# Optimization experiments

Measured on AMD Instinct MI355X. Metric: run time of the kernel, lower is better.

## Reference

```python
import jax, jax.numpy as jnp
import numpy as np

EMBED_DIM = 512
PAIR_DIM = 64
NUM_HEAD = 32
HEAD_DIM = EMBED_DIM // NUM_HEAD
LN_EPS = 1e-5


def layer_norm(x, gamma, beta):
    mu = jnp.mean(x, axis=-1, keepdims=True)
    var = jnp.var(x, axis=-1, keepdims=True)
    return (x - mu) * jax.lax.rsqrt(var + LN_EPS) * gamma + beta


def setup_inputs() -> dict:
    key = jax.random.key(0)
    ks = jax.random.split(key, 12)
    nc, n = 4, 512
    inp = {
        "query": jax.random.normal(ks[0], (nc, n, EMBED_DIM), dtype=jnp.float32),
        "pair": jax.random.normal(ks[1], (nc, n, n, PAIR_DIM), dtype=jnp.float32),
        "delta_pos": jax.random.normal(ks[2], (nc, n, n, 3), dtype=jnp.float32),
        # learned params
        "ln_q_g": jnp.ones((EMBED_DIM,), jnp.float32),
        "ln_q_b": jnp.zeros((EMBED_DIM,), jnp.float32),
        "ln_p_g": jnp.ones((PAIR_DIM,), jnp.float32),
        "ln_p_b": jnp.zeros((PAIR_DIM,), jnp.float32),
        # torch Linear weight layout [out, in]
        "Wq": jax.random.normal(ks[3], (EMBED_DIM, EMBED_DIM), jnp.float32) * (EMBED_DIM ** -0.5),
        "Wk": jax.random.normal(ks[4], (EMBED_DIM, EMBED_DIM), jnp.float32) * (EMBED_DIM ** -0.5),
        "Wv": jax.random.normal(ks[5], (EMBED_DIM, EMBED_DIM), jnp.float32) * (EMBED_DIM ** -0.5),
        "Wb": jax.random.normal(ks[6], (NUM_HEAD, PAIR_DIM), jnp.float32) * (PAIR_DIM ** -0.5),
        "bb": jnp.zeros((NUM_HEAD,), jnp.float32),
        # force_proj uses 'final' init (zeros); use small random so grads are nontrivial
        "Wf": jax.random.normal(ks[7], (1, EMBED_DIM), jnp.float32) * (EMBED_DIM ** -0.5),
    }
    return inp


def reference(query, pair, delta_pos, ln_q_g, ln_q_b, ln_p_g, ln_p_b, Wq, Wk, Wv, Wb, bb, Wf):
    nc, n, _ = query.shape
    H, D = NUM_HEAD, HEAD_DIM
    scaling = D ** -0.5

    xq = layer_norm(query, ln_q_g, ln_q_b)           # [c, n, E]
    xp = layer_norm(pair, ln_p_g, ln_p_b)            # [c, n, n, P]

    q = (xq @ Wq.T).reshape(nc, n, H, D).transpose(0, 2, 1, 3) * scaling  # [c,h,n,d]
    k = (xq @ Wk.T).reshape(nc, n, H, D).transpose(0, 2, 1, 3)            # [c,h,n,d]
    v = (xq @ Wv.T).reshape(nc, n, H, D).transpose(0, 2, 1, 3)            # [c,h,n,d]

    attn = jnp.einsum('chid,chjd->chij', q, k)                            # [c,h,n,n]
    bias = jnp.einsum('cijp,hp->chij', xp, Wb) + bb[None, :, None, None]  # [c,h,n,n]
    probs = jax.nn.softmax(attn + bias, axis=-1)  # dropout omitted (eval mode)

    # x[c,i,r,h,d] = sum_j probs[c,h,i,j] * delta_pos[c,i,j,r] * v[c,h,j,d]
    x = jnp.einsum('chij,cijr,chjd->cirhd', probs, delta_pos, v)
    x = x.reshape(nc, n, 3, H * D)                                        # [c,n,3,E]
    force = jnp.einsum('cire,e->cir', x, Wf[0])                           # [c,n,3]
    return force
```

## Files before the change

kernel.cpp:

```cpp
#include <hip/hip_runtime.h>
#include <hip/hip_bf16.h>
#include <math.h>

#define NN 512
#define HH 32
#define PP 64
#define EE 512

__global__ __launch_bounds__(256)
void prep_kernel(const float* __restrict__ Wv, const float* __restrict__ Wf,
                 const float* __restrict__ Wb, const float* __restrict__ pg,
                 const float* __restrict__ pb, const float* __restrict__ bbv,
                 float* __restrict__ Wu, float* __restrict__ Wbp,
                 float* __restrict__ s1, float* __restrict__ s2) {
    const int h = blockIdx.x;
    const int t = threadIdx.x;
    __shared__ float sh1[64], sh2[64];
#pragma unroll
    for (int r = 0; r < 2; ++r) {
        const int e = r * 256 + t;
        float acc = 0.f;
#pragma unroll
        for (int d = 0; d < 16; ++d)
            acc += Wf[h * 16 + d] * Wv[(size_t)(h * 16 + d) * EE + e];
        Wu[h * EE + e] = acc;
    }
    if (t < 64) {
        const float wb = Wb[h * PP + t];
        Wbp[h * PP + t] = pg[t] * wb;
        sh1[t] = pg[t] * wb;
        sh2[t] = pb[t] * wb;
    }
    __syncthreads();
    if (t == 0) {
        float a = 0.f, s = 0.f;
#pragma unroll
        for (int p = 0; p < 64; ++p) { a += sh1[p]; s += sh2[p]; }
        s1[h] = a;
        s2[h] = s + bbv[h];
    }
}

__global__ __launch_bounds__(256)
void ln_query_kernel(const float* __restrict__ x, const float* __restrict__ g,
                     const float* __restrict__ b, float* __restrict__ xq) {
    const int row = blockIdx.x;
    const int t = threadIdx.x;
    const int wave = t >> 6, lane = t & 63;
    const float2 v = ((const float2*)(x + (size_t)row * EE))[t];
    float s = v.x + v.y;
    float ss = v.x * v.x + v.y * v.y;
#pragma unroll
    for (int o = 32; o > 0; o >>= 1) {
        s += __shfl_xor(s, o, 64);
        ss += __shfl_xor(ss, o, 64);
    }
    __shared__ float rs[4], rss[4];
    if (lane == 0) { rs[wave] = s; rss[wave] = ss; }
    __syncthreads();
    s = rs[0] + rs[1] + rs[2] + rs[3];
    ss = rss[0] + rss[1] + rss[2] + rss[3];
    const float mu = s * (1.f / 512.f);
    const float var = ss * (1.f / 512.f) - mu * mu;
    const float istd = rsqrtf(var + 1e-5f);
    const float2 gg = ((const float2*)g)[t];
    const float2 bb2 = ((const float2*)b)[t];
    float2 o;
    o.x = (v.x - mu) * istd * gg.x + bb2.x;
    o.y = (v.y - mu) * istd * gg.y + bb2.y;
    ((float2*)(xq + (size_t)row * EE))[t] = o;
}

__global__ __launch_bounds__(256)
void proj_gemm_kernel(const float* __restrict__ xq, const float* __restrict__ Wq,
                      const float* __restrict__ Wk, const float* __restrict__ Wu,
                      float* __restrict__ qo, float* __restrict__ kt,
                      float* __restrict__ uT) {
    __shared__ float As[32][33];
    __shared__ float Bs[32][33];
    const int t = threadIdx.x;
    const int row0 = blockIdx.x * 32;
    const int col0 = blockIdx.y * 32;
    const int tx = t & 15, ty = t >> 4;
    const int lr = t >> 3;
    const int lk4 = (t & 7) * 4;

    const int gcb = col0 + lr;
    const float* wrow;
    if (gcb < 512) wrow = Wq + (size_t)gcb * EE;
    else if (gcb < 1024) wrow = Wk + (size_t)(gcb - 512) * EE;
    else wrow = Wu + (size_t)(gcb - 1024) * EE;
    const float* arow = xq + (size_t)(row0 + lr) * EE;

    float a00 = 0.f, a01 = 0.f, a10 = 0.f, a11 = 0.f;
#pragma unroll 1
    for (int k0 = 0; k0 < EE; k0 += 32) {
        const float4 av = *(const float4*)(arow + k0 + lk4);
        const float4 bv = *(const float4*)(wrow + k0 + lk4);
        __syncthreads();
        As[lk4 + 0][lr] = av.x; As[lk4 + 1][lr] = av.y;
        As[lk4 + 2][lr] = av.z; As[lk4 + 3][lr] = av.w;
        Bs[lk4 + 0][lr] = bv.x; Bs[lk4 + 1][lr] = bv.y;
        Bs[lk4 + 2][lr] = bv.z; Bs[lk4 + 3][lr] = bv.w;
        __syncthreads();
#pragma unroll
        for (int kk = 0; kk < 32; ++kk) {
            const float2 a = *(const float2*)&As[kk][ty * 2];
            const float2 b = *(const float2*)&Bs[kk][tx * 2];
            a00 += a.x * b.x; a01 += a.x * b.y;
            a10 += a.y * b.x; a11 += a.y * b.y;
        }
    }

    float accv[2][2] = {{a00, a01}, {a10, a11}};
#pragma unroll
    for (int r = 0; r < 2; ++r) {
        const int grow = row0 + ty * 2 + r;
        const int c = grow >> 9, n = grow & 511;
#pragma unroll
        for (int cc = 0; cc < 2; ++cc) {
            const int gc = col0 + tx * 2 + cc;
            const float v = accv[r][cc];
            if (gc < 512) {
                qo[(size_t)grow * EE + gc] = v * 0.25f;
            } else if (gc < 1024) {
                const int e = gc - 512;
                const int h = e >> 4, d = e & 15;
                kt[((((size_t)c * HH + h) * 8 + (d >> 1)) * NN + n) * 2 + (d & 1)] = v;
            } else {
                const int h = gc - 1024;
                uT[((size_t)c * HH + h) * NN + n] = v;
            }
        }
    }
}

__global__ __launch_bounds__(512)
void attn_force_kernel(const float* __restrict__ pair, const float* __restrict__ delta,
                       const float* __restrict__ qws, const float* __restrict__ kt,
                       const float* __restrict__ uT, const float* __restrict__ Wbp,
                       const float* __restrict__ s1, const float* __restrict__ s2,
                       float* __restrict__ out) {
    __shared__ float attn[HH][NN];
    __shared__ float invd[HH];
    __shared__ float red[8][3];

    const int t = threadIdx.x;
    const int wave = t >> 6, lane = t & 63;
    const int bid = blockIdx.x;
    const int c = bid >> 9;
    const int i = bid & 511;
    const int j = t;

    const float4* prow = (const float4*)(pair + (((size_t)c * NN + i) * NN + j) * PP);
    const float* qrow = qws + (size_t)bid * EE;
    const float2* ktc = (const float2*)(kt + (size_t)c * HH * 8 * NN * 2);

    float mu = 0.f, istd = 0.f;
#pragma unroll 1
    for (int g = 0; g < 4; ++g) {
        float l8[8] = {0.f, 0.f, 0.f, 0.f, 0.f, 0.f, 0.f, 0.f};
        float s = 0.f, ss = 0.f;
#pragma unroll
        for (int x = 0; x < 16; ++x) {
            const float4 pv = prow[x];
            if (g == 0) {
                s += pv.x + pv.y + pv.z + pv.w;
                ss += pv.x * pv.x + pv.y * pv.y + pv.z * pv.z + pv.w * pv.w;
            }
#pragma unroll
            for (int hh = 0; hh < 8; ++hh) {
                const float4 w = *(const float4*)(Wbp + (g * 8 + hh) * PP + x * 4);
                l8[hh] += pv.x * w.x + pv.y * w.y + pv.z * w.z + pv.w * w.w;
            }
        }
        if (g == 0) {
            mu = s * (1.f / 64.f);
            const float var = ss * (1.f / 64.f) - mu * mu;
            istd = rsqrtf(var + 1e-5f);
        }
#pragma unroll
        for (int hh = 0; hh < 8; ++hh) {
            const int h = g * 8 + hh;
            float qk = 0.f;
#pragma unroll
            for (int dp = 0; dp < 8; ++dp) {
                const float2 kv = ktc[((size_t)h * 8 + dp) * NN + j];
                const float2 qv = *(const float2*)(qrow + h * 16 + dp * 2);
                qk += kv.x * qv.x + kv.y * qv.y;
            }
            attn[h][j] = __expf(qk + istd * (l8[hh] - mu * s1[h]) + s2[h]);
        }
    }
    __syncthreads();

#pragma unroll
    for (int q = 0; q < 4; ++q) {
        const int h = wave * 4 + q;
        float v = 0.f;
#pragma unroll
        for (int x = 0; x < 8; ++x) v += attn[h][x * 64 + lane];
#pragma unroll
        for (int o = 32; o > 0; o >>= 1) v += __shfl_xor(v, o, 64);
        if (lane == 0) invd[h] = 1.f / v;
    }
    __syncthreads();

    float w = 0.f;
#pragma unroll
    for (int h = 0; h < HH; ++h)
        w += attn[h][j] * invd[h] * uT[((size_t)c * HH + h) * NN + j];

    const float* d3 = delta + (((size_t)c * NN + i) * NN + j) * 3;
    float fx = w * d3[0], fy = w * d3[1], fz = w * d3[2];
#pragma unroll
    for (int o = 32; o > 0; o >>= 1) {
        fx += __shfl_xor(fx, o, 64);
        fy += __shfl_xor(fy, o, 64);
        fz += __shfl_xor(fz, o, 64);
    }
    if (lane == 0) { red[wave][0] = fx; red[wave][1] = fy; red[wave][2] = fz; }
    __syncthreads();
    if (t == 0) {
        float ox = 0.f, oy = 0.f, oz = 0.f;
#pragma unroll
        for (int w8 = 0; w8 < 8; ++w8) { ox += red[w8][0]; oy += red[w8][1]; oz += red[w8][2]; }
        out[(size_t)bid * 3 + 0] = ox;
        out[(size_t)bid * 3 + 1] = oy;
        out[(size_t)bid * 3 + 2] = oz;
    }
}

extern "C" void kernel_launch(void* const* d_in, const int* in_sizes, int n_in,
                              void* d_out, int out_size, void* d_ws, size_t ws_size,
                              hipStream_t stream) {
    const float* query   = (const float*)d_in[0];
    const float* pair    = (const float*)d_in[1];
    const float* delta   = (const float*)d_in[2];
    const float* ln_q_g  = (const float*)d_in[3];
    const float* ln_q_b  = (const float*)d_in[4];
    const float* ln_p_g  = (const float*)d_in[5];
    const float* ln_p_b  = (const float*)d_in[6];
    const float* Wq      = (const float*)d_in[7];
    const float* Wk      = (const float*)d_in[8];
    const float* Wv      = (const float*)d_in[9];
    const float* Wb      = (const float*)d_in[10];
    const float* bbv     = (const float*)d_in[11];
    const float* Wf      = (const float*)d_in[12];
    float* out = (float*)d_out;

    float* ws = (float*)d_ws;
    float* xq  = ws;
    float* qws = xq + 2048 * 512;
    float* kt  = qws + 2048 * 512;
    float* uT  = kt + 2048 * 512;
    float* Wu  = uT + 4 * 32 * 512;
    float* Wbp = Wu + 32 * 512;
    float* s1  = Wbp + 32 * 64;
    float* s2  = s1 + 32;

    prep_kernel<<<32, 256, 0, stream>>>(Wv, Wf, Wb, ln_p_g, ln_p_b, bbv,
                                        Wu, Wbp, s1, s2);
    ln_query_kernel<<<2048, 256, 0, stream>>>(query, ln_q_g, ln_q_b, xq);
    proj_gemm_kernel<<<dim3(64, 33), 256, 0, stream>>>(xq, Wq, Wk, Wu,
                                                       qws, kt, uT);
    attn_force_kernel<<<2048, 512, 0, stream>>>(pair, delta, qws, kt, uT,
                                                Wbp, s1, s2, out);
}
```

Before: 590.6 us.

## Keep attention exponentials in registers and relayout K for float4 loads

The per-row attention exponentials now stay in a 32-entry register array, so the 64 KB shared-memory attention buffer is gone. The softmax denominator is built with wave shuffles and a small per-wave partial table. K is rewritten as contiguous 16-float rows per (head, key) so each thread can read it with four float4 loads, and the group loop is fully unrolled with a launch-bounds occupancy hint. The aim is higher occupancy from lower LDS use. The cost is more register pressure, and K reads are now strided across lanes (64 bytes apart), which may hurt coalescing.

Measured after the change: 1.898 ms. 221% more time.

```diff
diff --git a/kernel.cpp b/kernel.cpp
--- a/kernel.cpp
+++ b/kernel.cpp
@@ -74,7 +74,7 @@
 __global__ __launch_bounds__(256)
 void proj_gemm_kernel(const float* __restrict__ xq, const float* __restrict__ Wq,
                       const float* __restrict__ Wk, const float* __restrict__ Wu,
-                      float* __restrict__ qo, float* __restrict__ kt,
+                      float* __restrict__ qo, float* __restrict__ ktn,
                       float* __restrict__ uT) {
     __shared__ float As[32][33];
     __shared__ float Bs[32][33];
@@ -126,7 +126,7 @@
             } else if (gc < 1024) {
                 const int e = gc - 512;
                 const int h = e >> 4, d = e & 15;
-                kt[((((size_t)c * HH + h) * 8 + (d >> 1)) * NN + n) * 2 + (d & 1)] = v;
+                ktn[(((size_t)c * HH + h) * NN + n) * 16 + d] = v;
             } else {
                 const int h = gc - 1024;
                 uT[((size_t)c * HH + h) * NN + n] = v;
@@ -135,13 +135,13 @@
     }
 }
 
-__global__ __launch_bounds__(512)
+__global__ __launch_bounds__(512, 4)
 void attn_force_kernel(const float* __restrict__ pair, const float* __restrict__ delta,
-                       const float* __restrict__ qws, const float* __restrict__ kt,
+                       const float* __restrict__ qws, const float* __restrict__ ktn,
                        const float* __restrict__ uT, const float* __restrict__ Wbp,
                        const float* __restrict__ s1, const float* __restrict__ s2,
                        float* __restrict__ out) {
-    __shared__ float attn[HH][NN];
+    __shared__ float part[HH][8];
     __shared__ float invd[HH];
     __shared__ float red[8][3];
 
@@ -154,13 +154,15 @@
 
     const float4* prow = (const float4*)(pair + (((size_t)c * NN + i) * NN + j) * PP);
     const float* qrow = qws + (size_t)bid * EE;
-    const float2* ktc = (const float2*)(kt + (size_t)c * HH * 8 * NN * 2);
-
+    const float* ktb = ktn + (size_t)c * HH * NN * 16;
+
+    float e32[32];
     float mu = 0.f, istd = 0.f;
-#pragma unroll 1
+    float s = 0.f, ss = 0.f;
+
+#pragma unroll
     for (int g = 0; g < 4; ++g) {
         float l8[8] = {0.f, 0.f, 0.f, 0.f, 0.f, 0.f, 0.f, 0.f};
-        float s = 0.f, ss = 0.f;
 #pragma unroll
         for (int x = 0; x < 16; ++x) {
             const float4 pv = prow[x];
@@ -170,8 +172,8 @@
             }
 #pragma unroll
             for (int hh = 0; hh < 8; ++hh) {
-                const float4 w = *(const float4*)(Wbp + (g * 8 + hh) * PP + x * 4);
-                l8[hh] += pv.x * w.x + pv.y * w.y + pv.z * w.z + pv.w * w.w;
+                const float4 wv = *(const float4*)(Wbp + (g * 8 + hh) * PP + x * 4);
+                l8[hh] += pv.x * wv.x + pv.y * wv.y + pv.z * wv.z + pv.w * wv.w;
             }
         }
         if (g == 0) {
@@ -182,34 +184,41 @@
 #pragma unroll
         for (int hh = 0; hh < 8; ++hh) {
             const int h = g * 8 + hh;
-            float qk = 0.f;
-#pragma unroll
-            for (int dp = 0; dp < 8; ++dp) {
-                const float2 kv = ktc[((size_t)h * 8 + dp) * NN + j];
-                const float2 qv = *(const float2*)(qrow + h * 16 + dp * 2);
-                qk += kv.x * qv.x + kv.y * qv.y;
-            }
-            attn[h][j] = __expf(qk + istd * (l8[hh] - mu * s1[h]) + s2[h]);
-        }
-    }
-    __syncthreads();
-
-#pragma unroll
-    for (int q = 0; q < 4; ++q) {
-        const int h = wave * 4 + q;
-        float v = 0.f;
-#pragma unroll
-        for (int x = 0; x < 8; ++x) v += attn[h][x * 64 + lane];
+            const float4* kv = (const float4*)(ktb + ((size_t)h * NN + j) * 16);
+            const float4 k0 = kv[0], k1 = kv[1], k2 = kv[2], k3 = kv[3];
+            const float4 q0 = *(const float4*)(qrow + h * 16 + 0);
+            const float4 q1 = *(const float4*)(qrow + h * 16 + 4);
+            const float4 q2 = *(const float4*)(qrow + h * 16 + 8);
+            const float4 q3 = *(const float4*)(qrow + h * 16 + 12);
+            float qk = k0.x * q0.x + k0.y * q0.y + k0.z * q0.z + k0.w * q0.w;
+            qk += k1.x * q1.x + k1.y * q1.y + k1.z * q1.z + k1.w * q1.w;
+            qk += k2.x * q2.x + k2.y * q2.y + k2.z * q2.z + k2.w * q2.w;
+            qk += k3.x * q3.x + k3.y * q3.y + k3.z * q3.z + k3.w * q3.w;
+            e32[h] = __expf(qk + istd * (l8[hh] - mu * s1[h]) + s2[h]);
+        }
+    }
+
+#pragma unroll
+    for (int h = 0; h < HH; ++h) {
+        float v = e32[h];
 #pragma unroll
         for (int o = 32; o > 0; o >>= 1) v += __shfl_xor(v, o, 64);
-        if (lane == 0) invd[h] = 1.f / v;
+        if (lane == 0) part[h][wave] = v;
+    }
+    __syncthreads();
+    if (t < HH) {
+        float d = 0.f;
+#pragma unroll
+        for (int w8 = 0; w8 < 8; ++w8) d += part[t][w8];
+        invd[t] = 1.f / d;
     }
     __syncthreads();
 
     float w = 0.f;
+    const float* urow = uT + (size_t)c * HH * NN + j;
 #pragma unroll
     for (int h = 0; h < HH; ++h)
-        w += attn[h][j] * invd[h] * uT[((size_t)c * HH + h) * NN + j];
+        w += e32[h] * invd[h] * urow[(size_t)h * NN];
 
     const float* d3 = delta + (((size_t)c * NN + i) * NN + j) * 3;
     float fx = w * d3[0], fy = w * d3[1], fz = w * d3[2];
@@ -252,8 +261,8 @@
     float* ws = (float*)d_ws;
     float* xq  = ws;
     float* qws = xq + 2048 * 512;
-    float* kt  = qws + 2048 * 512;
-    float* uT  = kt + 2048 * 512;
+    float* ktn = qws + 2048 * 512;
+    float* uT  = ktn + 2048 * 512;
     float* Wu  = uT + 4 * 32 * 512;
     float* Wbp = Wu + 32 * 512;
     float* s1  = Wbp + 32 * 64;
@@ -263,7 +272,7 @@
                                         Wu, Wbp, s1, s2);
     ln_query_kernel<<<2048, 256, 0, stream>>>(query, ln_q_g, ln_q_b, xq);
     proj_gemm_kernel<<<dim3(64, 33), 256, 0, stream>>>(xq, Wq, Wk, Wu,
-                                                       qws, kt, uT);
-    attn_force_kernel<<<2048, 512, 0, stream>>>(pair, delta, qws, kt, uT,
+                                                       qws, ktn, uT);
+    attn_force_kernel<<<2048, 512, 0, stream>>>(pair, delta, qws, ktn, uT,
                                                 Wbp, s1, s2, out);
 }
```
